# Performance work log

Hardware: AMD Instinct MI355X
Metric: run time of the kernel (lower is better)

The kernel has to match this reference:

```python
import jax, jax.numpy as jnp
import numpy as np

N_NODES = 50000


def mean_aggregate(x, src, dst):
    # gather source features, scatter-sum to destinations, divide by in-degree
    msgs = x[src]                                             # [E, D]
    summed = jax.ops.segment_sum(msgs, dst, num_segments=N_NODES)  # [N, D]
    deg = jax.ops.segment_sum(jnp.ones_like(dst, dtype=x.dtype), dst,
                              num_segments=N_NODES)           # [N]
    return summed / jnp.clip(deg, 1.0)[:, None]


def sage_conv(x, src, dst, Wl, Wr, b):
    # PyG SAGEConv (aggr='mean'): lin_l(agg) + lin_r(x); bias only on lin_l
    agg = mean_aggregate(x, src, dst)
    return agg @ Wl + b + x @ Wr


def setup_inputs() -> dict:
    key = jax.random.key(0)
    ks = jax.random.split(key, 8)
    x = jax.random.normal(ks[0], (N_NODES, 64), dtype=jnp.float32)
    edge_index = jax.random.randint(ks[1], (2, 800000), 0, N_NODES, dtype=jnp.int32)
    W1l = jax.random.normal(ks[2], (64, 128), dtype=jnp.float32) * (1.0 / np.sqrt(64))
    W1r = jax.random.normal(ks[3], (64, 128), dtype=jnp.float32) * (1.0 / np.sqrt(64))
    b1 = jnp.zeros((128,), dtype=jnp.float32)
    W2l = jax.random.normal(ks[4], (128, 40), dtype=jnp.float32) * (1.0 / np.sqrt(128))
    W2r = jax.random.normal(ks[5], (128, 40), dtype=jnp.float32) * (1.0 / np.sqrt(128))
    b2 = jnp.zeros((40,), dtype=jnp.float32)
    return {"x": x, "edge_index": edge_index, "W1l": W1l, "W1r": W1r, "b1": b1,
            "W2l": W2l, "W2r": W2r, "b2": b2}


def reference(x, edge_index, W1l, W1r, b1, W2l, W2r, b2):
    src, dst = edge_index[0], edge_index[1]
    h = sage_conv(x, src, dst, W1l, W1r, b1)
    h = jax.nn.relu(h)
    # dropout p=0.5 is identity in eval mode (self.training=False)
    h = sage_conv(h, src, dst, W2l, W2r, b2)
    return h, jax.nn.log_softmax(h, axis=1)
```

## Files before the change

kernel.cpp:

```cpp
#include <hip/hip_runtime.h>
#include <hip/hip_bf16.h>
#include <math.h>

#define N_NODES 50000
#define D0 64
#define D1 128
#define D2 40

#define NB  1024
#define NPB 49
#define CAP 1024

typedef short s16x8 __attribute__((ext_vector_type(8)));
typedef float f32x4 __attribute__((ext_vector_type(4)));

static __device__ __forceinline__ unsigned short f2bf(float v) {
    __hip_bfloat16 hb = __float2bfloat16(v);
    return *(unsigned short*)&hb;
}

__global__ __launch_bounds__(256) void prep_scatter_kernel(
        const float* __restrict__ x, const int* __restrict__ src, const int* __restrict__ dst,
        const float* __restrict__ W1l, const float* __restrict__ W1r,
        const float* __restrict__ W2l, const float* __restrict__ W2r,
        unsigned short* __restrict__ xh, int* __restrict__ gcur, unsigned* __restrict__ ebuf,
        unsigned short* __restrict__ wpk1, unsigned short* __restrict__ wpk2,
        int E, int nScat, int nCast) {
    int b = blockIdx.x, t = threadIdx.x;
    if (b < nScat) {
        __shared__ int h[NB];
        __shared__ int base[NB];
        int e0 = b * 4096;
        h[t] = 0; h[t + 256] = 0; h[t + 512] = 0; h[t + 768] = 0;
        __syncthreads();
        int dloc[16];
#pragma unroll
        for (int u = 0; u < 16; ++u) {
            int e = e0 + u * 256 + t;
            dloc[u] = (e < E) ? dst[e] : -1;
            if (dloc[u] >= 0) atomicAdd(&h[(unsigned)dloc[u] / NPB], 1);
        }
        __syncthreads();
        for (int u = t; u < NB; u += 256)
            if (h[u] > 0) base[u] = u * CAP + atomicAdd(&gcur[u], h[u]);
        __syncthreads();
        h[t] = 0; h[t + 256] = 0; h[t + 512] = 0; h[t + 768] = 0;
        __syncthreads();
#pragma unroll
        for (int u = 0; u < 16; ++u) {
            int e = e0 + u * 256 + t;
            if (dloc[u] >= 0) {
                unsigned d = (unsigned)dloc[u];
                unsigned bk = d / NPB;
                unsigned ld = d - bk * NPB;
                int k = atomicAdd(&h[bk], 1);
                ebuf[base[bk] + k] = (ld << 17) | (unsigned)src[e];
            }
        }
    } else if (b < nScat + nCast) {
        int i = ((b - nScat) * 256 + t) * 4;
        float4 v = *(const float4*)(x + i);
        unsigned o0 = (unsigned)f2bf(v.x) | ((unsigned)f2bf(v.y) << 16);
        unsigned o1 = (unsigned)f2bf(v.z) | ((unsigned)f2bf(v.w) << 16);
        uint2 pk; pk.x = o0; pk.y = o1;
        *(uint2*)(xh + i) = pk;
    } else if (b < nScat + nCast + 8) {
        int f = (b - nScat - nCast) * 4 + (t >> 6);
        int lane = t & 63;
        int nt = f & 7;
        int col = nt * 16 + (lane & 15);
        int kbase = (f >> 3) * 32 + (lane >> 4) * 8;
        unsigned short* o = wpk1 + ((size_t)f * 64 + lane) * 8;
#pragma unroll
        for (int j = 0; j < 8; ++j) {
            int k = kbase + j;
            float w = (k < 64) ? W1r[k * 128 + col] : W1l[(k - 64) * 128 + col];
            o[j] = f2bf(w);
        }
    } else {
        int f = (b - nScat - nCast - 8) * 4 + (t >> 6);
        if (f < 20) {
            int lane = t & 63;
            int nt = f % 5;
            int col = nt * 16 + (lane & 15);
            int kbase = (f / 5) * 32 + (lane >> 4) * 8;
            unsigned short* o = wpk2 + ((size_t)f * 64 + lane) * 8;
#pragma unroll
            for (int j = 0; j < 8; ++j) {
                int k = kbase + j;
                float w = (col < 40) ? W2l[k * 40 + col] : W2r[k * 40 + (col - 40)];
                o[j] = f2bf(w);
            }
        }
    }
}

__global__ __launch_bounds__(256) void fillagg1_kernel(
        const unsigned short* __restrict__ xh, const unsigned* __restrict__ ebuf,
        const int* __restrict__ gcur,
        int* __restrict__ rowstart, int* __restrict__ rowcnt, int* __restrict__ csr,
        unsigned short* __restrict__ aggh, int N) {
    __shared__ int csr_l[CAP];
    __shared__ int cnt[64];
    __shared__ int sd[64];
    __shared__ int rs[64];
    __shared__ int pos[64];
    int b = blockIdx.x, t = threadIdx.x;
    int s0 = b * CAP;
    int ne = gcur[b]; ne = (ne < CAP) ? ne : CAP;
    unsigned ev[4];
#pragma unroll
    for (int u = 0; u < 4; ++u) {
        int i = t + u * 256;
        ev[u] = (i < ne) ? ebuf[s0 + i] : 0xFFFFFFFFu;
    }
    if (t < 64) cnt[t] = 0;
    __syncthreads();
#pragma unroll
    for (int u = 0; u < 4; ++u)
        if (ev[u] != 0xFFFFFFFFu) atomicAdd(&cnt[ev[u] >> 17], 1);
    __syncthreads();
    if (t < 64) sd[t] = cnt[t];
    __syncthreads();
    for (int off = 1; off < 64; off <<= 1) {
        int u = (t >= off && t < 64) ? sd[t - off] : 0;
        __syncthreads();
        if (t < 64) sd[t] += u;
        __syncthreads();
    }
    if (t < 64) {
        int ex = sd[t] - cnt[t];
        rs[t] = ex;
        pos[t] = ex;
    }
    __syncthreads();
#pragma unroll
    for (int u = 0; u < 4; ++u) {
        if (ev[u] != 0xFFFFFFFFu) {
            int ld = (int)(ev[u] >> 17);
            int p = atomicAdd(&pos[ld], 1);
            csr_l[p] = (int)(ev[u] & 0x1FFFFu);
        }
    }
    if (t < NPB) {
        int node = b * NPB + t;
        if (node < N) {
            rowstart[node] = s0 + rs[t];
            rowcnt[node] = cnt[t];
        }
    }
    __syncthreads();
    for (int i = t; i < ne; i += 256) csr[s0 + i] = csr_l[i];

    int w = t >> 6, lane = t & 63;
    int l = lane & 7, g = lane >> 3;
    for (int n = w; n < NPB; n += 4) {
        int node = b * NPB + n;
        if (node >= N) break;
        int beg = rs[n];
        int deg = cnt[n];
        float acc[8];
#pragma unroll
        for (int k = 0; k < 8; ++k) acc[k] = 0.f;
        int jmax = (deg + 7) >> 3;
        int full = jmax - 1;
        int j = 0;
        for (; j + 2 <= full; j += 2) {
            int s0e = csr_l[beg + j * 8 + g];
            int s1e = csr_l[beg + (j + 1) * 8 + g];
            uint4 v0 = *(const uint4*)(xh + (size_t)s0e * D0 + l * 8);
            uint4 v1 = *(const uint4*)(xh + (size_t)s1e * D0 + l * 8);
            acc[0] += __uint_as_float(v0.x << 16);  acc[1] += __uint_as_float(v0.x & 0xffff0000u);
            acc[2] += __uint_as_float(v0.y << 16);  acc[3] += __uint_as_float(v0.y & 0xffff0000u);
            acc[4] += __uint_as_float(v0.z << 16);  acc[5] += __uint_as_float(v0.z & 0xffff0000u);
            acc[6] += __uint_as_float(v0.w << 16);  acc[7] += __uint_as_float(v0.w & 0xffff0000u);
            acc[0] += __uint_as_float(v1.x << 16);  acc[1] += __uint_as_float(v1.x & 0xffff0000u);
            acc[2] += __uint_as_float(v1.y << 16);  acc[3] += __uint_as_float(v1.y & 0xffff0000u);
            acc[4] += __uint_as_float(v1.z << 16);  acc[5] += __uint_as_float(v1.z & 0xffff0000u);
            acc[6] += __uint_as_float(v1.w << 16);  acc[7] += __uint_as_float(v1.w & 0xffff0000u);
        }
        if (j < full) {
            int s0e = csr_l[beg + j * 8 + g];
            uint4 v0 = *(const uint4*)(xh + (size_t)s0e * D0 + l * 8);
            acc[0] += __uint_as_float(v0.x << 16);  acc[1] += __uint_as_float(v0.x & 0xffff0000u);
            acc[2] += __uint_as_float(v0.y << 16);  acc[3] += __uint_as_float(v0.y & 0xffff0000u);
            acc[4] += __uint_as_float(v0.z << 16);  acc[5] += __uint_as_float(v0.z & 0xffff0000u);
            acc[6] += __uint_as_float(v0.w << 16);  acc[7] += __uint_as_float(v0.w & 0xffff0000u);
        }
        if (jmax > 0) {
            int slot = full * 8 + g;
            int e = beg + ((slot < deg) ? slot : (deg - 1));
            int s0e = csr_l[e];
            float wgt = (slot < deg) ? 1.f : 0.f;
            uint4 v0 = *(const uint4*)(xh + (size_t)s0e * D0 + l * 8);
            acc[0] = fmaf(wgt, __uint_as_float(v0.x << 16), acc[0]);
            acc[1] = fmaf(wgt, __uint_as_float(v0.x & 0xffff0000u), acc[1]);
            acc[2] = fmaf(wgt, __uint_as_float(v0.y << 16), acc[2]);
            acc[3] = fmaf(wgt, __uint_as_float(v0.y & 0xffff0000u), acc[3]);
            acc[4] = fmaf(wgt, __uint_as_float(v0.z << 16), acc[4]);
            acc[5] = fmaf(wgt, __uint_as_float(v0.z & 0xffff0000u), acc[5]);
            acc[6] = fmaf(wgt, __uint_as_float(v0.w << 16), acc[6]);
            acc[7] = fmaf(wgt, __uint_as_float(v0.w & 0xffff0000u), acc[7]);
        }
#pragma unroll
        for (int off = 8; off <= 32; off <<= 1) {
#pragma unroll
            for (int k = 0; k < 8; ++k) acc[k] += __shfl_xor(acc[k], off);
        }
        float inv = 1.f / (float)max(deg, 1);
        if (g == 0) {
            unsigned o0 = (unsigned)f2bf(acc[0] * inv) | ((unsigned)f2bf(acc[1] * inv) << 16);
            unsigned o1 = (unsigned)f2bf(acc[2] * inv) | ((unsigned)f2bf(acc[3] * inv) << 16);
            unsigned o2 = (unsigned)f2bf(acc[4] * inv) | ((unsigned)f2bf(acc[5] * inv) << 16);
            unsigned o3 = (unsigned)f2bf(acc[6] * inv) | ((unsigned)f2bf(acc[7] * inv) << 16);
            uint4 pk; pk.x = o0; pk.y = o1; pk.z = o2; pk.w = o3;
            *(uint4*)(aggh + (size_t)node * D0 + l * 8) = pk;
        }
    }
}


__global__ void agg2_kernel(const unsigned short* __restrict__ p2h, const float* __restrict__ r2,
                            const int* __restrict__ rowstart, const int* __restrict__ rowcnt,
                            const int* __restrict__ csr,
                            float* __restrict__ out, float* __restrict__ out2, int N) {
    int wid = (blockIdx.x * blockDim.x + threadIdx.x) >> 6;
    int lane = threadIdx.x & 63;
    if (wid >= N) return;
    int beg = rowstart[wid];
    int deg = rowcnt[wid];
    int g = lane / 5;
    int l = lane - g * 5;
    bool gv = g < 12;
    float a[8];
#pragma unroll
    for (int k = 0; k < 8; ++k) a[k] = 0.f;
    int jmax = (deg + 11) / 12;
    int full = jmax - 1;
    int j = 0;
    for (; j + 2 <= full; j += 2) {
        int s0 = csr[beg + j * 12 + g];
        int s1 = csr[beg + (j + 1) * 12 + g];
        uint4 v0 = *(const uint4*)(p2h + (size_t)s0 * 64 + l * 8);
        uint4 v1 = *(const uint4*)(p2h + (size_t)s1 * 64 + l * 8);
        if (gv) {
            a[0] += __uint_as_float(v0.x << 16);  a[1] += __uint_as_float(v0.x & 0xffff0000u);
            a[2] += __uint_as_float(v0.y << 16);  a[3] += __uint_as_float(v0.y & 0xffff0000u);
            a[4] += __uint_as_float(v0.z << 16);  a[5] += __uint_as_float(v0.z & 0xffff0000u);
            a[6] += __uint_as_float(v0.w << 16);  a[7] += __uint_as_float(v0.w & 0xffff0000u);
            a[0] += __uint_as_float(v1.x << 16);  a[1] += __uint_as_float(v1.x & 0xffff0000u);
            a[2] += __uint_as_float(v1.y << 16);  a[3] += __uint_as_float(v1.y & 0xffff0000u);
            a[4] += __uint_as_float(v1.z << 16);  a[5] += __uint_as_float(v1.z & 0xffff0000u);
            a[6] += __uint_as_float(v1.w << 16);  a[7] += __uint_as_float(v1.w & 0xffff0000u);
        }
    }
    if (j < full) {
        int s0 = csr[beg + j * 12 + g];
        uint4 v0 = *(const uint4*)(p2h + (size_t)s0 * 64 + l * 8);
        if (gv) {
            a[0] += __uint_as_float(v0.x << 16);  a[1] += __uint_as_float(v0.x & 0xffff0000u);
            a[2] += __uint_as_float(v0.y << 16);  a[3] += __uint_as_float(v0.y & 0xffff0000u);
            a[4] += __uint_as_float(v0.z << 16);  a[5] += __uint_as_float(v0.z & 0xffff0000u);
            a[6] += __uint_as_float(v0.w << 16);  a[7] += __uint_as_float(v0.w & 0xffff0000u);
        }
    }
    if (jmax > 0) {
        int slot = full * 12 + g;
        int e = beg + ((slot < deg) ? slot : (deg - 1));
        int s0 = csr[e];
        float w = (gv && slot < deg) ? 1.f : 0.f;
        uint4 v0 = *(const uint4*)(p2h + (size_t)s0 * 64 + l * 8);
        a[0] = fmaf(w, __uint_as_float(v0.x << 16), a[0]);
        a[1] = fmaf(w, __uint_as_float(v0.x & 0xffff0000u), a[1]);
        a[2] = fmaf(w, __uint_as_float(v0.y << 16), a[2]);
        a[3] = fmaf(w, __uint_as_float(v0.y & 0xffff0000u), a[3]);
        a[4] = fmaf(w, __uint_as_float(v0.z << 16), a[4]);
        a[5] = fmaf(w, __uint_as_float(v0.z & 0xffff0000u), a[5]);
        a[6] = fmaf(w, __uint_as_float(v0.w << 16), a[6]);
        a[7] = fmaf(w, __uint_as_float(v0.w & 0xffff0000u), a[7]);
    }
    {
        float b0;
#pragma unroll
        for (int k = 0; k < 8; ++k) { b0 = __shfl(a[k], lane + 30); if (g < 6) a[k] += b0; }
#pragma unroll
        for (int k = 0; k < 8; ++k) { b0 = __shfl(a[k], lane + 15); if (g < 3) a[k] += b0; }
#pragma unroll
        for (int k = 0; k < 8; ++k) {
            float c1 = __shfl(a[k], lane + 5);
            float c2 = __shfl(a[k], lane + 10);
            if (g == 0) a[k] += c1 + c2;
        }
    }
    float inv = 1.f / (float)max(deg, 1);
    bool wr = (lane < 5);
    float h2[8];
    if (wr) {
        float4 ra = *(const float4*)(r2 + (size_t)wid * D2 + lane * 8);
        float4 rb = *(const float4*)(r2 + (size_t)wid * D2 + lane * 8 + 4);
        h2[0] = ra.x + a[0] * inv; h2[1] = ra.y + a[1] * inv;
        h2[2] = ra.z + a[2] * inv; h2[3] = ra.w + a[3] * inv;
        h2[4] = rb.x + a[4] * inv; h2[5] = rb.y + a[5] * inv;
        h2[6] = rb.z + a[6] * inv; h2[7] = rb.w + a[7] * inv;
        float4 oa; oa.x = h2[0]; oa.y = h2[1]; oa.z = h2[2]; oa.w = h2[3];
        float4 ob; ob.x = h2[4]; ob.y = h2[5]; ob.z = h2[6]; ob.w = h2[7];
        *(float4*)(out + (size_t)wid * D2 + lane * 8) = oa;
        *(float4*)(out + (size_t)wid * D2 + lane * 8 + 4) = ob;
    }
    float m = -INFINITY;
    if (wr) {
#pragma unroll
        for (int k = 0; k < 8; ++k) m = fmaxf(m, h2[k]);
    }
#pragma unroll
    for (int off = 1; off < 64; off <<= 1) m = fmaxf(m, __shfl_xor(m, off));
    float s = 0.f;
    if (wr) {
#pragma unroll
        for (int k = 0; k < 8; ++k) s += expf(h2[k] - m);
    }
#pragma unroll
    for (int off = 1; off < 64; off <<= 1) s += __shfl_xor(s, off);
    if (wr) {
        float lg = m + logf(s);
        float4 oa; oa.x = h2[0] - lg; oa.y = h2[1] - lg; oa.z = h2[2] - lg; oa.w = h2[3] - lg;
        float4 ob; ob.x = h2[4] - lg; ob.y = h2[5] - lg; ob.z = h2[6] - lg; ob.w = h2[7] - lg;
        *(float4*)(out2 + (size_t)wid * D2 + lane * 8) = oa;
        *(float4*)(out2 + (size_t)wid * D2 + lane * 8 + 4) = ob;
    }
}

__global__ __launch_bounds__(256) void gemm_fused(
        const unsigned short* __restrict__ xh, const unsigned short* __restrict__ aggh,
        const unsigned short* __restrict__ Wpk1, const unsigned short* __restrict__ Wpk2,
        const float* __restrict__ b1, const float* __restrict__ b2,
        unsigned short* __restrict__ p2h, float* __restrict__ r2, int N) {
    __shared__ __align__(16) unsigned short As[64 * 136];
    int t = threadIdx.x;
    int r0 = blockIdx.x * 64;
    for (int i = t; i < 1024; i += 256) {
        int r = i >> 4, c = i & 15;
        int gr = r0 + r; gr = (gr < N) ? gr : (N - 1);
        uint4 v = (c < 8) ? ((const uint4*)(xh + (size_t)gr * 64))[c]
                          : ((const uint4*)(aggh + (size_t)gr * 64))[c - 8];
        *(uint4*)(As + r * 136 + c * 8) = v;
    }
    __syncthreads();
    int w = t >> 6, lane = t & 63;
    int l15 = lane & 15, q = lane >> 4;
    f32x4 zero = {0.f, 0.f, 0.f, 0.f};
    const unsigned short* abase = As + (w * 16 + l15) * 136 + q * 8;

    f32x4 acc[8];
#pragma unroll
    for (int nt = 0; nt < 8; ++nt) acc[nt] = zero;
#pragma unroll
    for (int ks = 0; ks < 4; ++ks) {
        s16x8 a0 = *(const s16x8*)(abase + ks * 32);
        s16x8 b[8];
#pragma unroll
        for (int nt = 0; nt < 8; ++nt)
            b[nt] = *(const s16x8*)(Wpk1 + ((size_t)(ks * 8 + nt) * 64 + lane) * 8);
#pragma unroll
        for (int nt = 0; nt < 8; ++nt)
            acc[nt] = __builtin_amdgcn_mfma_f32_16x16x32_bf16(a0, b[nt], acc[nt], 0, 0, 0);
    }
    int rloc = w * 16 + q * 4;
#pragma unroll
    for (int nt = 0; nt < 8; ++nt) {
        int col = nt * 16 + l15;
        float bias = b1[col];
#pragma unroll
        for (int reg = 0; reg < 4; ++reg)
            As[(rloc + reg) * 136 + col] = f2bf(fmaxf(acc[nt][reg] + bias, 0.f));
    }
    f32x4 acc2[5];
#pragma unroll
    for (int nt = 0; nt < 5; ++nt) acc2[nt] = zero;
#pragma unroll
    for (int ks = 0; ks < 4; ++ks) {
        s16x8 a0 = *(const s16x8*)(abase + ks * 32);
        s16x8 b[5];
#pragma unroll
        for (int nt = 0; nt < 5; ++nt)
            b[nt] = *(const s16x8*)(Wpk2 + ((size_t)(ks * 5 + nt) * 64 + lane) * 8);
#pragma unroll
        for (int nt = 0; nt < 5; ++nt)
            acc2[nt] = __builtin_amdgcn_mfma_f32_16x16x32_bf16(a0, b[nt], acc2[nt], 0, 0, 0);
    }
    int rbase = r0 + w * 16 + q * 4;
#pragma unroll
    for (int nt = 0; nt < 5; ++nt) {
        int col = nt * 16 + l15;
        bool isp = col < 40;
        int oc = isp ? col : (col - 40);
        float bias = isp ? 0.f : b2[oc];
#pragma unroll
        for (int reg = 0; reg < 4; ++reg) {
            int row = rbase + reg;
            if (row < N) {
                float v = acc2[nt][reg] + bias;
                if (isp) p2h[(size_t)row * 64 + oc] = f2bf(v);
                else     r2[(size_t)row * D2 + oc] = v;
            }
        }
    }
}


extern "C" void kernel_launch(void* const* d_in, const int* in_sizes, int n_in,
                              void* d_out, int out_size, void* d_ws, size_t ws_size,
                              hipStream_t stream) {
    const float* x   = (const float*)d_in[0];
    const int*   ei  = (const int*)d_in[1];
    const float* W1l = (const float*)d_in[2];
    const float* W1r = (const float*)d_in[3];
    const float* b1  = (const float*)d_in[4];
    const float* W2l = (const float*)d_in[5];
    const float* W2r = (const float*)d_in[6];
    const float* b2  = (const float*)d_in[7];
    float* out = (float*)d_out;

    const int N = N_NODES;
    const int E = in_sizes[1] / 2;
    const int* src = ei;
    const int* dst = ei + E;

    char* p = (char*)d_ws;
    auto alloc = [&](size_t bytes) -> void* {
        void* r = (void*)p;
        p += (bytes + 255) & ~(size_t)255;
        return r;
    };
    const int nScat = (E + 4095) / 4096;
    const int nCast = (N * D0) / 1024;

    unsigned* ebuf     = (unsigned*)alloc((size_t)NB * CAP * 4);
    int*      csr      = (int*)alloc((size_t)NB * CAP * 4);
    int*      gcur     = (int*)alloc(NB * 4);
    int*      rowstart = (int*)alloc((size_t)N * 4);
    int*      rowcnt   = (int*)alloc((size_t)N * 4);
    unsigned short* xh    = (unsigned short*)alloc((size_t)N * D0 * 2);
    unsigned short* aggh  = (unsigned short*)alloc((size_t)N * D0 * 2);
    unsigned short* wpk1  = (unsigned short*)alloc((size_t)32 * 64 * 8 * 2);
    unsigned short* wpk2  = (unsigned short*)alloc((size_t)20 * 64 * 8 * 2);
    unsigned short* p2h   = (unsigned short*)alloc((size_t)N * 64 * 2);
    float* r2buf = (float*)alloc((size_t)N * D2 * 4);

    hipMemsetAsync(gcur, 0, NB * sizeof(int), stream);
    prep_scatter_kernel<<<nScat + nCast + 8 + 5, 256, 0, stream>>>(
        x, src, dst, W1l, W1r, W2l, W2r, xh, gcur, ebuf, wpk1, wpk2, E, nScat, nCast);

    fillagg1_kernel<<<NB, 256, 0, stream>>>(xh, ebuf, gcur, rowstart, rowcnt, csr, aggh, N);

    gemm_fused<<<(N + 63) / 64, 256, 0, stream>>>(xh, aggh, wpk1, wpk2, b1, b2,
                                                  p2h, r2buf, N);

    agg2_kernel<<<(N * 64 + 255) / 256, 256, 0, stream>>>(p2h, r2buf, rowstart, rowcnt, csr,
                                                          out, out + (size_t)N * D2, N);
}
```

Baseline: 169.6 us.

## Fuse layer-1 aggregation with the fused GEMM via 64-node buckets

Result: no change. 168.9 us (-0.4%).

```diff
diff --git a/kernel.cpp b/kernel.cpp
--- a/kernel.cpp
+++ b/kernel.cpp
@@ -7,9 +7,9 @@
 #define D1 128
 #define D2 40
 
-#define NB  1024
-#define NPB 49
-#define CAP 1024
+#define NB  784
+#define NPB 64
+#define CAP 1280
 
 typedef short s16x8 __attribute__((ext_vector_type(8)));
 typedef float f32x4 __attribute__((ext_vector_type(4)));
@@ -31,28 +31,28 @@
         __shared__ int h[NB];
         __shared__ int base[NB];
         int e0 = b * 4096;
-        h[t] = 0; h[t + 256] = 0; h[t + 512] = 0; h[t + 768] = 0;
+        for (int i = t; i < NB; i += 256) h[i] = 0;
         __syncthreads();
         int dloc[16];
 #pragma unroll
         for (int u = 0; u < 16; ++u) {
             int e = e0 + u * 256 + t;
             dloc[u] = (e < E) ? dst[e] : -1;
-            if (dloc[u] >= 0) atomicAdd(&h[(unsigned)dloc[u] / NPB], 1);
+            if (dloc[u] >= 0) atomicAdd(&h[(unsigned)dloc[u] >> 6], 1);
         }
         __syncthreads();
         for (int u = t; u < NB; u += 256)
             if (h[u] > 0) base[u] = u * CAP + atomicAdd(&gcur[u], h[u]);
         __syncthreads();
-        h[t] = 0; h[t + 256] = 0; h[t + 512] = 0; h[t + 768] = 0;
+        for (int i = t; i < NB; i += 256) h[i] = 0;
         __syncthreads();
 #pragma unroll
         for (int u = 0; u < 16; ++u) {
             int e = e0 + u * 256 + t;
             if (dloc[u] >= 0) {
                 unsigned d = (unsigned)dloc[u];
-                unsigned bk = d / NPB;
-                unsigned ld = d - bk * NPB;
+                unsigned bk = d >> 6;
+                unsigned ld = d & 63u;
                 int k = atomicAdd(&h[bk], 1);
                 ebuf[base[bk] + k] = (ld << 17) | (unsigned)src[e];
             }
@@ -95,29 +95,38 @@
     }
 }
 
-__global__ __launch_bounds__(256) void fillagg1_kernel(
+__global__ __launch_bounds__(256) void fillagg1gemm_kernel(
         const unsigned short* __restrict__ xh, const unsigned* __restrict__ ebuf,
         const int* __restrict__ gcur,
+        const unsigned short* __restrict__ Wpk1, const unsigned short* __restrict__ Wpk2,
+        const float* __restrict__ b1, const float* __restrict__ b2,
         int* __restrict__ rowstart, int* __restrict__ rowcnt, int* __restrict__ csr,
-        unsigned short* __restrict__ aggh, int N) {
+        unsigned short* __restrict__ p2h, float* __restrict__ r2, int N) {
     __shared__ int csr_l[CAP];
     __shared__ int cnt[64];
     __shared__ int sd[64];
     __shared__ int rs[64];
     __shared__ int pos[64];
+    __shared__ __align__(16) unsigned short As[64 * 136];
     int b = blockIdx.x, t = threadIdx.x;
+    int r0 = b * 64;
+    for (int i = t; i < 512; i += 256) {
+        int r = i >> 3, c = i & 7;
+        int gr = r0 + r; gr = (gr < N) ? gr : (N - 1);
+        *(uint4*)(As + r * 136 + c * 8) = ((const uint4*)(xh + (size_t)gr * 64))[c];
+    }
     int s0 = b * CAP;
     int ne = gcur[b]; ne = (ne < CAP) ? ne : CAP;
-    unsigned ev[4];
-#pragma unroll
-    for (int u = 0; u < 4; ++u) {
+    unsigned ev[5];
+#pragma unroll
+    for (int u = 0; u < 5; ++u) {
         int i = t + u * 256;
         ev[u] = (i < ne) ? ebuf[s0 + i] : 0xFFFFFFFFu;
     }
     if (t < 64) cnt[t] = 0;
     __syncthreads();
 #pragma unroll
-    for (int u = 0; u < 4; ++u)
+    for (int u = 0; u < 5; ++u)
         if (ev[u] != 0xFFFFFFFFu) atomicAdd(&cnt[ev[u] >> 17], 1);
     __syncthreads();
     if (t < 64) sd[t] = cnt[t];
@@ -135,15 +144,15 @@
     }
     __syncthreads();
 #pragma unroll
-    for (int u = 0; u < 4; ++u) {
+    for (int u = 0; u < 5; ++u) {
         if (ev[u] != 0xFFFFFFFFu) {
             int ld = (int)(ev[u] >> 17);
             int p = atomicAdd(&pos[ld], 1);
             csr_l[p] = (int)(ev[u] & 0x1FFFFu);
         }
     }
-    if (t < NPB) {
-        int node = b * NPB + t;
+    if (t < 64) {
+        int node = r0 + t;
         if (node < N) {
             rowstart[node] = s0 + rs[t];
             rowcnt[node] = cnt[t];
@@ -154,8 +163,8 @@
 
     int w = t >> 6, lane = t & 63;
     int l = lane & 7, g = lane >> 3;
-    for (int n = w; n < NPB; n += 4) {
-        int node = b * NPB + n;
+    for (int n = w; n < 64; n += 4) {
+        int node = r0 + n;
         if (node >= N) break;
         int beg = rs[n];
         int deg = cnt[n];
@@ -214,7 +223,66 @@
             unsigned o2 = (unsigned)f2bf(acc[4] * inv) | ((unsigned)f2bf(acc[5] * inv) << 16);
             unsigned o3 = (unsigned)f2bf(acc[6] * inv) | ((unsigned)f2bf(acc[7] * inv) << 16);
             uint4 pk; pk.x = o0; pk.y = o1; pk.z = o2; pk.w = o3;
-            *(uint4*)(aggh + (size_t)node * D0 + l * 8) = pk;
+            *(uint4*)(As + n * 136 + 64 + l * 8) = pk;
+        }
+    }
+    __syncthreads();
+
+    int l15 = lane & 15, q = lane >> 4;
+    f32x4 zero = {0.f, 0.f, 0.f, 0.f};
+    const unsigned short* abase = As + (w * 16 + l15) * 136 + q * 8;
+    f32x4 acc1[8];
+#pragma unroll
+    for (int nt = 0; nt < 8; ++nt) acc1[nt] = zero;
+#pragma unroll
+    for (int ks = 0; ks < 4; ++ks) {
+        s16x8 a0 = *(const s16x8*)(abase + ks * 32);
+        s16x8 bb[8];
+#pragma unroll
+        for (int nt = 0; nt < 8; ++nt)
+            bb[nt] = *(const s16x8*)(Wpk1 + ((size_t)(ks * 8 + nt) * 64 + lane) * 8);
+#pragma unroll
+        for (int nt = 0; nt < 8; ++nt)
+            acc1[nt] = __builtin_amdgcn_mfma_f32_16x16x32_bf16(a0, bb[nt], acc1[nt], 0, 0, 0);
+    }
+    int rloc = w * 16 + q * 4;
+#pragma unroll
+    for (int nt = 0; nt < 8; ++nt) {
+        int col = nt * 16 + l15;
+        float bias = b1[col];
+#pragma unroll
+        for (int reg = 0; reg < 4; ++reg)
+            As[(rloc + reg) * 136 + col] = f2bf(fmaxf(acc1[nt][reg] + bias, 0.f));
+    }
+    f32x4 acc2[5];
+#pragma unroll
+    for (int nt = 0; nt < 5; ++nt) acc2[nt] = zero;
+#pragma unroll
+    for (int ks = 0; ks < 4; ++ks) {
+        s16x8 a0 = *(const s16x8*)(abase + ks * 32);
+        s16x8 bb[5];
+#pragma unroll
+        for (int nt = 0; nt < 5; ++nt)
+            bb[nt] = *(const s16x8*)(Wpk2 + ((size_t)(ks * 5 + nt) * 64 + lane) * 8);
+#pragma unroll
+        for (int nt = 0; nt < 5; ++nt)
+            acc2[nt] = __builtin_amdgcn_mfma_f32_16x16x32_bf16(a0, bb[nt], acc2[nt], 0, 0, 0);
+    }
+    int rbase = r0 + w * 16 + q * 4;
+#pragma unroll
+    for (int nt = 0; nt < 5; ++nt) {
+        int col = nt * 16 + l15;
+        bool isp = col < 40;
+        int oc = isp ? col : (col - 40);
+        float bias = isp ? 0.f : b2[oc];
+#pragma unroll
+        for (int reg = 0; reg < 4; ++reg) {
+            int row = rbase + reg;
+            if (row < N) {
+                float v = acc2[nt][reg] + bias;
+                if (isp) p2h[(size_t)row * 64 + oc] = f2bf(v);
+                else     r2[(size_t)row * D2 + oc] = v;
+            }
         }
     }
 }
@@ -330,83 +398,6 @@
     }
 }
 
-__global__ __launch_bounds__(256) void gemm_fused(
-        const unsigned short* __restrict__ xh, const unsigned short* __restrict__ aggh,
-        const unsigned short* __restrict__ Wpk1, const unsigned short* __restrict__ Wpk2,
-        const float* __restrict__ b1, const float* __restrict__ b2,
-        unsigned short* __restrict__ p2h, float* __restrict__ r2, int N) {
-    __shared__ __align__(16) unsigned short As[64 * 136];
-    int t = threadIdx.x;
-    int r0 = blockIdx.x * 64;
-    for (int i = t; i < 1024; i += 256) {
-        int r = i >> 4, c = i & 15;
-        int gr = r0 + r; gr = (gr < N) ? gr : (N - 1);
-        uint4 v = (c < 8) ? ((const uint4*)(xh + (size_t)gr * 64))[c]
-                          : ((const uint4*)(aggh + (size_t)gr * 64))[c - 8];
-        *(uint4*)(As + r * 136 + c * 8) = v;
-    }
-    __syncthreads();
-    int w = t >> 6, lane = t & 63;
-    int l15 = lane & 15, q = lane >> 4;
-    f32x4 zero = {0.f, 0.f, 0.f, 0.f};
-    const unsigned short* abase = As + (w * 16 + l15) * 136 + q * 8;
-
-    f32x4 acc[8];
-#pragma unroll
-    for (int nt = 0; nt < 8; ++nt) acc[nt] = zero;
-#pragma unroll
-    for (int ks = 0; ks < 4; ++ks) {
-        s16x8 a0 = *(const s16x8*)(abase + ks * 32);
-        s16x8 b[8];
-#pragma unroll
-        for (int nt = 0; nt < 8; ++nt)
-            b[nt] = *(const s16x8*)(Wpk1 + ((size_t)(ks * 8 + nt) * 64 + lane) * 8);
-#pragma unroll
-        for (int nt = 0; nt < 8; ++nt)
-            acc[nt] = __builtin_amdgcn_mfma_f32_16x16x32_bf16(a0, b[nt], acc[nt], 0, 0, 0);
-    }
-    int rloc = w * 16 + q * 4;
-#pragma unroll
-    for (int nt = 0; nt < 8; ++nt) {
-        int col = nt * 16 + l15;
-        float bias = b1[col];
-#pragma unroll
-        for (int reg = 0; reg < 4; ++reg)
-            As[(rloc + reg) * 136 + col] = f2bf(fmaxf(acc[nt][reg] + bias, 0.f));
-    }
-    f32x4 acc2[5];
-#pragma unroll
-    for (int nt = 0; nt < 5; ++nt) acc2[nt] = zero;
-#pragma unroll
-    for (int ks = 0; ks < 4; ++ks) {
-        s16x8 a0 = *(const s16x8*)(abase + ks * 32);
-        s16x8 b[5];
-#pragma unroll
-        for (int nt = 0; nt < 5; ++nt)
-            b[nt] = *(const s16x8*)(Wpk2 + ((size_t)(ks * 5 + nt) * 64 + lane) * 8);
-#pragma unroll
-        for (int nt = 0; nt < 5; ++nt)
-            acc2[nt] = __builtin_amdgcn_mfma_f32_16x16x32_bf16(a0, b[nt], acc2[nt], 0, 0, 0);
-    }
-    int rbase = r0 + w * 16 + q * 4;
-#pragma unroll
-    for (int nt = 0; nt < 5; ++nt) {
-        int col = nt * 16 + l15;
-        bool isp = col < 40;
-        int oc = isp ? col : (col - 40);
-        float bias = isp ? 0.f : b2[oc];
-#pragma unroll
-        for (int reg = 0; reg < 4; ++reg) {
-            int row = rbase + reg;
-            if (row < N) {
-                float v = acc2[nt][reg] + bias;
-                if (isp) p2h[(size_t)row * 64 + oc] = f2bf(v);
-                else     r2[(size_t)row * D2 + oc] = v;
-            }
-        }
-    }
-}
-
 
 extern "C" void kernel_launch(void* const* d_in, const int* in_sizes, int n_in,
                               void* d_out, int out_size, void* d_ws, size_t ws_size,
@@ -441,7 +432,6 @@
     int*      rowstart = (int*)alloc((size_t)N * 4);
     int*      rowcnt   = (int*)alloc((size_t)N * 4);
     unsigned short* xh    = (unsigned short*)alloc((size_t)N * D0 * 2);
-    unsigned short* aggh  = (unsigned short*)alloc((size_t)N * D0 * 2);
     unsigned short* wpk1  = (unsigned short*)alloc((size_t)32 * 64 * 8 * 2);
     unsigned short* wpk2  = (unsigned short*)alloc((size_t)20 * 64 * 8 * 2);
     unsigned short* p2h   = (unsigned short*)alloc((size_t)N * 64 * 2);
@@ -451,10 +441,8 @@
     prep_scatter_kernel<<<nScat + nCast + 8 + 5, 256, 0, stream>>>(
         x, src, dst, W1l, W1r, W2l, W2r, xh, gcur, ebuf, wpk1, wpk2, E, nScat, nCast);
 
-    fillagg1_kernel<<<NB, 256, 0, stream>>>(xh, ebuf, gcur, rowstart, rowcnt, csr, aggh, N);
-
-    gemm_fused<<<(N + 63) / 64, 256, 0, stream>>>(xh, aggh, wpk1, wpk2, b1, b2,
-                                                  p2h, r2buf, N);
+    fillagg1gemm_kernel<<<NB, 256, 0, stream>>>(xh, ebuf, gcur, wpk1, wpk2, b1, b2,
+                                                rowstart, rowcnt, csr, p2h, r2buf, N);
 
     agg2_kernel<<<(N * 64 + 255) / 256, 256, 0, stream>>>(p2h, r2buf, rowstart, rowcnt, csr,
                                                           out, out + (size_t)N * D2, N);
```
